# Performance work log

Hardware: AMD Instinct MI355X
Metric: run time of the kernel (lower is better)

Reference implementation:

```python
import jax, jax.numpy as jnp
import numpy as np

B, H, L, N, COND = 8, 128, 16384, 16, 4  # N = s4_hidden_size // 2 complex states (conjugate symmetry)
BN_EPS = 1e-5


def setup_inputs() -> dict:
    key = jax.random.key(0)
    ks = jax.random.split(key, 12)
    x = jax.random.normal(ks[0], (B, H, L), jnp.float32)
    conditional_information = jax.random.normal(ks[1], (B, COND), jnp.float32)
    # input linear (H -> H)
    lin_w = jax.random.normal(ks[2], (H, H), jnp.float32) / np.sqrt(H)
    lin_b = jnp.zeros((H,), jnp.float32)
    prelu1_a = jnp.array(0.25, jnp.float32)
    # S4D (diag) parameters, ZOH discretization, S4D-Lin init
    u = jax.random.uniform(ks[3], (H,), jnp.float32)
    log_dt = np.log(1e-3) + u * (np.log(1e-1) - np.log(1e-3))  # [H]
    log_A_real = jnp.log(0.5 * jnp.ones((H, N), jnp.float32))
    A_imag = jnp.broadcast_to(np.pi * jnp.arange(N, dtype=jnp.float32), (H, N)).copy()
    C_re = jax.random.normal(ks[4], (H, N), jnp.float32)
    C_im = jax.random.normal(ks[5], (H, N), jnp.float32)
    D = jax.random.normal(ks[6], (H,), jnp.float32)
    out_w = jax.random.normal(ks[7], (H, H), jnp.float32) / np.sqrt(H)
    out_b = jnp.zeros((H,), jnp.float32)
    # FiLM: cond -> (gamma, beta) per channel
    film_w = jax.random.normal(ks[8], (2 * H, COND), jnp.float32) / np.sqrt(COND)
    film_b = jnp.zeros((2 * H,), jnp.float32)
    prelu2_a = jnp.array(0.25, jnp.float32)
    # depthwise 1x1 conv residual: per-channel scale
    res_w = jax.random.normal(ks[9], (H,), jnp.float32) / np.sqrt(H)
    return dict(x=x, conditional_information=conditional_information,
                lin_w=lin_w, lin_b=lin_b, prelu1_a=prelu1_a,
                log_dt=log_dt, log_A_real=log_A_real, A_imag=A_imag,
                C_re=C_re, C_im=C_im, D=D, out_w=out_w, out_b=out_b,
                film_w=film_w, film_b=film_b, prelu2_a=prelu2_a, res_w=res_w)


def _prelu(v, a):
    return jnp.where(v > 0, v, a * v)


def _s4d(u, log_dt, log_A_real, A_imag, C_re, C_im, D, out_w, out_b):
    # u: [B, H, L]. Diagonal SSM kernel via Vandermonde + FFT convolution (ZOH).
    Lx = u.shape[-1]
    dt = jnp.exp(log_dt)                                   # [H]
    A = -jnp.exp(log_A_real) + 1j * A_imag                 # [H, N] complex
    dtA = dt[:, None] * A                                  # [H, N]
    dB = (jnp.exp(dtA) - 1.0) / A                          # ZOH: (e^{dtA}-1)/A, B=1
    Ceff = (C_re + 1j * C_im) * dB                         # [H, N]
    t = jnp.arange(Lx, dtype=jnp.float32)
    vand = jnp.exp(dtA[:, :, None] * t)                    # [H, N, L] = (e^{dtA})^l
    K = 2.0 * jnp.real(jnp.einsum('hn,hnl->hl', Ceff, vand))  # [H, L]
    n = 2 * Lx
    y = jnp.fft.irfft(jnp.fft.rfft(u, n) * jnp.fft.rfft(K, n)[None], n)[..., :Lx]
    y = y + D[None, :, None] * u
    # position-wise output linear (activation='id')
    return jnp.einsum('bhl,gh->bgl', y, out_w) + out_b[None, :, None]


def reference(x, conditional_information, lin_w, lin_b, prelu1_a,
              log_dt, log_A_real, A_imag, C_re, C_im, D, out_w, out_b,
              film_w, film_b, prelu2_a, res_w):
    out = jnp.einsum('bhl,gh->bgl', x, lin_w) + lin_b[None, :, None]
    out = _prelu(out, prelu1_a)
    out = _s4d(out, log_dt, log_A_real, A_imag, C_re, C_im, D, out_w, out_b)
    # BatchNorm1d(affine=False), training-mode statistics over (B, L)
    mean = jnp.mean(out, axis=(0, 2), keepdims=True)
    var = jnp.var(out, axis=(0, 2), keepdims=True)
    out = (out - mean) * jax.lax.rsqrt(var + BN_EPS)
    # FiLM
    gb = conditional_information @ film_w.T + film_b       # [B, 2H]
    g, b = gb[:, :H], gb[:, H:]
    out = out * g[:, :, None] + b[:, :, None]
    out = _prelu(out, prelu2_a)
    # depthwise 1x1 conv residual (groups=H, no bias): per-channel scale of x
    return out + res_w[None, :, None] * x
```

## Files before the change

kernel.cpp:

```cpp
#include <hip/hip_runtime.h>
#include <math.h>

#define B_ 8
#define H_ 128
#define L_ 16384
#define N_ 16
#define CHUNK_ 64
#define NCH_ 256

typedef float f32x4 __attribute__((ext_vector_type(4)));
typedef short bf16x8 __attribute__((ext_vector_type(8)));

static __device__ __forceinline__ unsigned int f2bf(float f) {
  unsigned int u = __float_as_uint(f);
  return (u + 0x7FFFu + ((u >> 16) & 1u)) >> 16;
}
static __device__ __forceinline__ float bf2f(unsigned int us) {
  return __uint_as_float(us << 16);
}

__global__ __launch_bounds__(256) void prep2_kernel(
    const float* __restrict__ lin_w, const float* __restrict__ out_w,
    const float* __restrict__ log_dt, const float* __restrict__ log_A_real,
    const float* __restrict__ A_imag, const float* __restrict__ C_re,
    const float* __restrict__ C_im, const float* __restrict__ cond,
    const float* __restrict__ film_w, const float* __restrict__ film_b,
    unsigned short* __restrict__ wA16, unsigned short* __restrict__ wB16,
    float* __restrict__ consts,
    float* __restrict__ gact, float* __restrict__ bact)
{
  int blk = blockIdx.x, t = threadIdx.x;
  if (blk < 16) {
    int base = blk * 1024;
    #pragma unroll
    for (int it = 0; it < 4; it++) {
      int i = base + it * 256 + t;
      wA16[i] = (unsigned short)f2bf(lin_w[i]);
      wB16[i] = (unsigned short)f2bf(out_w[i]);
    }
  } else if (blk == 16) {
    for (int i = t; i < H_ * N_; i += 256) {
      int h = i >> 4, n = i & 15;
      float dt  = expf(log_dt[h]);
      float Are = -expf(log_A_real[i]);
      float Aim = A_imag[i];
      float dre = dt * Are, dim = dt * Aim;
      float er  = expf(dre);
      float wre = er * cosf(dim);
      float wim = er * sinf(dim);
      float den = Are * Are + Aim * Aim;
      float nre = wre - 1.0f, nim = wim;
      float dBre = (nre * Are + nim * Aim) / den;
      float dBim = (nim * Are - nre * Aim) / den;
      float cr = C_re[i], ci = C_im[i];
      float cere = cr * dBre - ci * dBim;
      float ceim = cr * dBim + ci * dBre;
      float e2   = expf((float)CHUNK_ * dre);
      float wcre = e2 * cosf((float)CHUNK_ * dim);
      float wcim = e2 * sinf((float)CHUNK_ * dim);
      float* cb = consts + h * 96;
      cb[n]      = wre;  cb[16 + n] = wim;
      cb[32 + n] = cere; cb[48 + n] = ceim;
      cb[64 + n] = wcre; cb[80 + n] = wcim;
    }
  } else {
    for (int i = t; i < B_ * 2 * H_; i += 256) {
      int b = i >> 8, k = i & 255;
      float acc = film_b[k];
      #pragma unroll
      for (int c = 0; c < 4; c++) acc += cond[b * 4 + c] * film_w[k * 4 + c];
      if (k < H_) gact[b * H_ + k] = acc;
      else        bact[b * H_ + (k - H_)] = acc;
    }
  }
}

template<int MODE>
__global__ __launch_bounds__(256) void mgemm_kernel(
    const void* inv, const unsigned short* __restrict__ w16,
    const float* __restrict__ bias, const float* __restrict__ prelu_a,
    unsigned short* __restrict__ outb)
{
  __shared__ __align__(16) unsigned short xT[64 * 128];
  char* xb = (char*)xT;
  int tid = threadIdx.x;
  int blk = blockIdx.x;
  int b   = blk >> 8;
  int jb  = (blk & 255) << 6;

  {
    int hp = tid >> 4;
    int jq = tid & 15;
    int h0 = hp << 3;
    if (MODE == 0) {
      const float* inb = (const float*)inv + ((size_t)b * H_) * L_ + jb;
      f32x4 r[8];
      #pragma unroll
      for (int rr = 0; rr < 8; rr++)
        r[rr] = *reinterpret_cast<const f32x4*>(&inb[(size_t)(h0 + rr) * L_ + (jq << 2)]);
      #pragma unroll
      for (int jj = 0; jj < 4; jj++) {
        int j = (jq << 2) + jj;
        uint4 pk;
        pk.x = f2bf(r[0][jj]) | (f2bf(r[1][jj]) << 16);
        pk.y = f2bf(r[2][jj]) | (f2bf(r[3][jj]) << 16);
        pk.z = f2bf(r[4][jj]) | (f2bf(r[5][jj]) << 16);
        pk.w = f2bf(r[6][jj]) | (f2bf(r[7][jj]) << 16);
        int addr = j * 256 + ((hp << 4) ^ ((j & 15) << 4));
        *reinterpret_cast<uint4*>(xb + addr) = pk;
      }
    } else {
      const unsigned short* ub = (const unsigned short*)inv;
      uint2 rv[8];
      #pragma unroll
      for (int rr = 0; rr < 8; rr++)
        rv[rr] = *reinterpret_cast<const uint2*>(
            ub + ((size_t)(b * H_ + h0 + rr)) * 32768 + jb + (jq << 2));
      #pragma unroll
      for (int jj = 0; jj < 4; jj++) {
        int j = (jq << 2) + jj;
        uint4 pk;
        #define EXT_(v) ((((jj & 2) ? (v).y : (v).x) >> ((jj & 1) << 4)) & 0xFFFFu)
        pk.x = EXT_(rv[0]) | (EXT_(rv[1]) << 16);
        pk.y = EXT_(rv[2]) | (EXT_(rv[3]) << 16);
        pk.z = EXT_(rv[4]) | (EXT_(rv[5]) << 16);
        pk.w = EXT_(rv[6]) | (EXT_(rv[7]) << 16);
        #undef EXT_
        int addr = j * 256 + ((hp << 4) ^ ((j & 15) << 4));
        *reinterpret_cast<uint4*>(xb + addr) = pk;
      }
    }
  }
  __syncthreads();

  int lane = tid & 63;
  int w    = tid >> 6;
  int wg   = w >> 1;
  int wj   = w & 1;
  int ln   = lane & 15;
  int q    = lane >> 4;
  f32x4 acc[4][2];
  #pragma unroll
  for (int mi = 0; mi < 4; mi++)
    #pragma unroll
    for (int n = 0; n < 2; n++) acc[mi][n] = (f32x4)0.0f;

  #pragma unroll
  for (int kb = 0; kb < 4; kb++) {
    bf16x8 a[4], bv[2];
    #pragma unroll
    for (int mi = 0; mi < 4; mi++)
      a[mi] = *reinterpret_cast<const bf16x8*>(
          &w16[(size_t)(wg * 64 + mi * 16 + ln) * 128 + kb * 32 + q * 8]);
    #pragma unroll
    for (int n = 0; n < 2; n++) {
      int jl = wj * 32 + n * 16 + ln;
      int ar = jl * 256 + (((kb << 6) + (q << 4)) ^ ((jl & 15) << 4));
      bv[n] = *reinterpret_cast<bf16x8*>(xb + ar);
    }
    #pragma unroll
    for (int mi = 0; mi < 4; mi++)
      #pragma unroll
      for (int n = 0; n < 2; n++)
        acc[mi][n] = __builtin_amdgcn_mfma_f32_16x16x32_bf16(a[mi], bv[n], acc[mi][n], 0, 0, 0);
  }

  float pa = (MODE == 0) ? prelu_a[0] : 0.0f;
  #pragma unroll
  for (int mi = 0; mi < 4; mi++) {
    #pragma unroll
    for (int r = 0; r < 4; r++) {
      int g = wg * 64 + mi * 16 + q * 4 + r;
      float bvs = bias[g];
      float v0 = acc[mi][0][r] + bvs;
      float v1 = acc[mi][1][r] + bvs;
      if (MODE == 0) {
        v0 = (v0 > 0.0f) ? v0 : pa * v0;
        v1 = (v1 > 0.0f) ? v1 : pa * v1;
      }
      size_t ob = ((size_t)(b * H_ + g)) * 32768 + jb + wj * 32 + ln;
      outb[ob]      = (unsigned short)f2bf(v0);
      outb[ob + 16] = (unsigned short)f2bf(v1);
    }
  }
}

__global__ __launch_bounds__(1024) void scan3_kernel(
    unsigned short* ub, const float* __restrict__ consts, const float* __restrict__ Dp)
{
  __shared__ unsigned int rowl[8192];
  __shared__ float st[NCH_ * 36];
  int tid = threadIdx.x;
  int row = blockIdx.x;
  int h   = row & 127;
  const float* cb = consts + h * 96;
  unsigned int* grow = (unsigned int*)ub + (size_t)row * 16384;

  #pragma unroll
  for (int rd = 0; rd < 2; rd++) {
    int u0  = rd * 4096 + tid * 4;
    uint4 v = *reinterpret_cast<const uint4*>(grow + u0);
    int x   = (u0 >> 5) & 31;
    int bse = u0 ^ (x & ~3);
    int pl  = x & 3;
    if (pl & 1) v = make_uint4(v.y, v.x, v.w, v.z);
    if (pl & 2) v = make_uint4(v.z, v.w, v.x, v.y);
    *reinterpret_cast<uint4*>(&rowl[bse]) = v;
  }
  __syncthreads();

  int c   = tid >> 2;
  int m   = tid & 3;
  int swz = c & 31;
  unsigned int* rc = rowl + c * 32;
  float* sc = st + c * 36 + m * 8;

  float wre[4], wim[4];
  #pragma unroll
  for (int k = 0; k < 4; k++) { wre[k] = cb[4*m+k]; wim[k] = cb[16+4*m+k]; }

  float sre[4] = {0.f,0.f,0.f,0.f}, sim[4] = {0.f,0.f,0.f,0.f};

  for (int e = 0; e < 32; e++) {
    unsigned int pv = rc[e ^ swz];
    float u0 = bf2f(pv & 0xFFFFu), u1 = bf2f(pv >> 16);
    #pragma unroll
    for (int k = 0; k < 4; k++) {
      float nr = fmaf(wre[k], sre[k], fmaf(-wim[k], sim[k], u0));
      float ni = fmaf(wre[k], sim[k], wim[k] * sre[k]);
      sre[k] = nr; sim[k] = ni;
    }
    #pragma unroll
    for (int k = 0; k < 4; k++) {
      float nr = fmaf(wre[k], sre[k], fmaf(-wim[k], sim[k], u1));
      float ni = fmaf(wre[k], sim[k], wim[k] * sre[k]);
      sre[k] = nr; sim[k] = ni;
    }
  }
  #pragma unroll
  for (int k = 0; k < 4; k++) { sc[2*k] = sre[k]; sc[2*k+1] = sim[k]; }
  __syncthreads();

  {
    float mre[4], mim[4];
    #pragma unroll
    for (int k = 0; k < 4; k++) { mre[k] = cb[64+4*m+k]; mim[k] = cb[80+4*m+k]; }
    for (int s = 0; s < 8; s++) {
      int off = 1 << s;
      float pr[4], pi[4];
      bool act = (c >= off);
      if (act) {
        const float* pc = st + (c - off) * 36 + m * 8;
        #pragma unroll
        for (int k = 0; k < 4; k++) { pr[k] = pc[2*k]; pi[k] = pc[2*k+1]; }
      }
      __syncthreads();
      if (act) {
        #pragma unroll
        for (int k = 0; k < 4; k++) {
          sre[k] = fmaf(mre[k], pr[k], fmaf(-mim[k], pi[k], sre[k]));
          sim[k] = fmaf(mre[k], pi[k], fmaf( mim[k], pr[k], sim[k]));
        }
        #pragma unroll
        for (int k = 0; k < 4; k++) { sc[2*k] = sre[k]; sc[2*k+1] = sim[k]; }
      }
      if (s < 7) {
        #pragma unroll
        for (int k = 0; k < 4; k++) {
          float r = mre[k], i2 = mim[k];
          mre[k] = r * r - i2 * i2;
          mim[k] = 2.0f * r * i2;
        }
      }
      __syncthreads();
    }
  }

  float cre[4], cim[4];
  #pragma unroll
  for (int k = 0; k < 4; k++) { cre[k] = cb[32+4*m+k]; cim[k] = cb[48+4*m+k]; }
  float Dv = Dp[h];
  if (c == 0) {
    #pragma unroll
    for (int k = 0; k < 4; k++) { sre[k] = 0.0f; sim[k] = 0.0f; }
  } else {
    const float* pc = st + (c - 1) * 36 + m * 8;
    #pragma unroll
    for (int k = 0; k < 4; k++) { sre[k] = pc[2*k]; sim[k] = pc[2*k+1]; }
  }
  for (int e = 0; e < 32; e++) {
    int p = e ^ swz;
    unsigned int pv = rc[p];
    float u0 = bf2f(pv & 0xFFFFu), u1 = bf2f(pv >> 16);
    float y0 = 0.0f, y1 = 0.0f;
    #pragma unroll
    for (int k = 0; k < 4; k++) {
      float nr = fmaf(wre[k], sre[k], fmaf(-wim[k], sim[k], u0));
      float ni = fmaf(wre[k], sim[k], wim[k] * sre[k]);
      sre[k] = nr; sim[k] = ni;
      y0 = fmaf(cre[k], nr, fmaf(-cim[k], ni, y0));
    }
    #pragma unroll
    for (int k = 0; k < 4; k++) {
      float nr = fmaf(wre[k], sre[k], fmaf(-wim[k], sim[k], u1));
      float ni = fmaf(wre[k], sim[k], wim[k] * sre[k]);
      sre[k] = nr; sim[k] = ni;
      y1 = fmaf(cre[k], nr, fmaf(-cim[k], ni, y1));
    }
    y0 += __shfl_xor(y0, 1); y0 += __shfl_xor(y0, 2);
    y1 += __shfl_xor(y1, 1); y1 += __shfl_xor(y1, 2);
    if (m == 0) {
      y0 = fmaf(Dv, u0, 2.0f * y0);
      y1 = fmaf(Dv, u1, 2.0f * y1);
      rc[p] = f2bf(y0) | (f2bf(y1) << 16);
    }
  }
  __syncthreads();

  #pragma unroll
  for (int rd = 0; rd < 2; rd++) {
    int u0  = rd * 4096 + tid * 4;
    int x   = (u0 >> 5) & 31;
    int bse = u0 ^ (x & ~3);
    int pl  = x & 3;
    uint4 v = *reinterpret_cast<const uint4*>(&rowl[bse]);
    if (pl & 1) v = make_uint4(v.y, v.x, v.w, v.z);
    if (pl & 2) v = make_uint4(v.z, v.w, v.x, v.y);
    *reinterpret_cast<uint4*>(grow + u0) = v;
  }
}

__global__ __launch_bounds__(256) void stats1_kernel(
    const unsigned short* __restrict__ ub,
    float* __restrict__ sums, float* __restrict__ sumsq)
{
  int row = blockIdx.x, tid = threadIdx.x;
  const unsigned int* zr = (const unsigned int*)ub + (size_t)row * 16384;
  float s1 = 0.0f, s2 = 0.0f;
  #pragma unroll
  for (int rd = 0; rd < 8; rd++) {
    uint4 v = *reinterpret_cast<const uint4*>(zr + rd * 1024 + tid * 4);
    unsigned int ws_[4] = {v.x, v.y, v.z, v.w};
    #pragma unroll
    for (int k = 0; k < 4; k++) {
      float f0 = bf2f(ws_[k] & 0xFFFFu), f1 = bf2f(ws_[k] >> 16);
      s1 += f0 + f1;
      s2 = fmaf(f0, f0, fmaf(f1, f1, s2));
    }
  }
  #pragma unroll
  for (int off = 1; off < 64; off <<= 1) {
    s1 += __shfl_xor(s1, off);
    s2 += __shfl_xor(s2, off);
  }
  __shared__ float a1[4], a2[4];
  int wv = tid >> 6;
  if ((tid & 63) == 0) { a1[wv] = s1; a2[wv] = s2; }
  __syncthreads();
  if (tid == 0) {
    sums[row]  = a1[0] + a1[1] + a1[2] + a1[3];
    sumsq[row] = a2[0] + a2[1] + a2[2] + a2[3];
  }
}

__global__ void stats2_kernel(const float* __restrict__ sums,
                              const float* __restrict__ sumsq,
                              float* __restrict__ meanp, float* __restrict__ invp)
{
  int g = threadIdx.x;
  if (g < H_) {
    double s1 = 0.0, s2 = 0.0;
    #pragma unroll
    for (int b = 0; b < B_; b++) {
      s1 += (double)sums[b * H_ + g];
      s2 += (double)sumsq[b * H_ + g];
    }
    double cnt = (double)B_ * (double)L_;
    double mu  = s1 / cnt;
    double var = s2 / cnt - mu * mu;
    meanp[g] = (float)mu;
    invp[g]  = (float)(1.0 / sqrt(var + 1e-5));
  }
}

__global__ __launch_bounds__(256) void final2_kernel(
    unsigned short* __restrict__ ub, float* __restrict__ outf,
    const float* __restrict__ x,
    const float* __restrict__ meanp, const float* __restrict__ invp,
    const float* __restrict__ gact, const float* __restrict__ bact,
    const float* __restrict__ prelu2_a, const float* __restrict__ res_w)
{
  int row = blockIdx.x, tid = threadIdx.x;
  int b = row >> 7, g = row & 127;
  const unsigned int* zr = (const unsigned int*)ub + (size_t)row * 16384;
  uint4 zq0 = *reinterpret_cast<const uint4*>(zr + 0 * 1024 + tid * 4);
  uint4 zq1 = *reinterpret_cast<const uint4*>(zr + 1 * 1024 + tid * 4);
  uint4 zq2 = *reinterpret_cast<const uint4*>(zr + 2 * 1024 + tid * 4);
  uint4 zq3 = *reinterpret_cast<const uint4*>(zr + 3 * 1024 + tid * 4);
  uint4 zq4 = *reinterpret_cast<const uint4*>(zr + 4 * 1024 + tid * 4);
  uint4 zq5 = *reinterpret_cast<const uint4*>(zr + 5 * 1024 + tid * 4);
  uint4 zq6 = *reinterpret_cast<const uint4*>(zr + 6 * 1024 + tid * 4);
  uint4 zq7 = *reinterpret_cast<const uint4*>(zr + 7 * 1024 + tid * 4);
  __syncthreads();

  float m  = meanp[g], iv = invp[g];
  float ga = gact[b * H_ + g], bb = bact[b * H_ + g];
  float rw = res_w[g], pa = prelu2_a[0];
  const float* xr = x + (size_t)row * L_;
  float* orow = outf + (size_t)row * L_;

  uint4 zqa[8] = {zq0, zq1, zq2, zq3, zq4, zq5, zq6, zq7};
  #pragma unroll
  for (int rd = 0; rd < 8; rd++) {
    int e0 = rd * 2048 + tid * 8;
    f32x4 x0 = *reinterpret_cast<const f32x4*>(xr + e0);
    f32x4 x1 = *reinterpret_cast<const f32x4*>(xr + e0 + 4);
    unsigned int wz[4] = {zqa[rd].x, zqa[rd].y, zqa[rd].z, zqa[rd].w};
    f32x4 o0, o1;
    #pragma unroll
    for (int k = 0; k < 4; k++) {
      float z0 = bf2f(wz[k] & 0xFFFFu), z1 = bf2f(wz[k] >> 16);
      float v0 = fmaf((z0 - m) * iv, ga, bb);
      float v1 = fmaf((z1 - m) * iv, ga, bb);
      v0 = (v0 > 0.0f) ? v0 : pa * v0;
      v1 = (v1 > 0.0f) ? v1 : pa * v1;
      float xa = (k < 2) ? x0[2 * k] : x1[2 * k - 4];
      float xbv = (k < 2) ? x0[2 * k + 1] : x1[2 * k - 3];
      float r0 = fmaf(rw, xa, v0);
      float r1 = fmaf(rw, xbv, v1);
      if (k < 2) { o0[2 * k] = r0; o0[2 * k + 1] = r1; }
      else       { o1[2 * k - 4] = r0; o1[2 * k - 3] = r1; }
    }
    *reinterpret_cast<f32x4*>(orow + e0)     = o0;
    *reinterpret_cast<f32x4*>(orow + e0 + 4) = o1;
  }
}

extern "C" void kernel_launch(void* const* d_in, const int* in_sizes, int n_in,
                              void* d_out, int out_size, void* d_ws, size_t ws_size,
                              hipStream_t stream)
{
  const float* x        = (const float*)d_in[0];
  const float* cond     = (const float*)d_in[1];
  const float* lin_w    = (const float*)d_in[2];
  const float* lin_b    = (const float*)d_in[3];
  const float* prelu1_a = (const float*)d_in[4];
  const float* log_dt   = (const float*)d_in[5];
  const float* log_A    = (const float*)d_in[6];
  const float* A_imag   = (const float*)d_in[7];
  const float* C_re     = (const float*)d_in[8];
  const float* C_im     = (const float*)d_in[9];
  const float* Dp       = (const float*)d_in[10];
  const float* out_w    = (const float*)d_in[11];
  const float* out_b    = (const float*)d_in[12];
  const float* film_w   = (const float*)d_in[13];
  const float* film_b   = (const float*)d_in[14];
  const float* prelu2_a = (const float*)d_in[15];
  const float* res_w    = (const float*)d_in[16];
  float* outf = (float*)d_out;
  unsigned short* ubuf = (unsigned short*)d_out;

  char* wsb = (char*)d_ws;
  float* consts         = (float*)(wsb + 0);
  unsigned short* wA16  = (unsigned short*)(wsb + 49152);
  unsigned short* wB16  = (unsigned short*)(wsb + 81920);
  float* gact           = (float*)(wsb + 114688);
  float* bact           = (float*)(wsb + 118784);
  float* meanp          = (float*)(wsb + 122880);
  float* invp           = (float*)(wsb + 123392);
  float* sums           = (float*)(wsb + 123904);
  float* sumsq          = (float*)(wsb + 128000);

  prep2_kernel<<<18, 256, 0, stream>>>(lin_w, out_w, log_dt, log_A, A_imag, C_re, C_im,
                                       cond, film_w, film_b, wA16, wB16, consts, gact, bact);
  mgemm_kernel<0><<<2048, 256, 0, stream>>>(x, wA16, lin_b, prelu1_a, ubuf);
  scan3_kernel<<<1024, 1024, 0, stream>>>(ubuf, consts, Dp);
  mgemm_kernel<1><<<2048, 256, 0, stream>>>(ubuf, wB16, out_b, nullptr, ubuf);
  stats1_kernel<<<1024, 256, 0, stream>>>(ubuf, sums, sumsq);
  stats2_kernel<<<1, 128, 0, stream>>>(sums, sumsq, meanp, invp);
  final2_kernel<<<1024, 256, 0, stream>>>(ubuf, outf, x, meanp, invp, gact, bact,
                                          prelu2_a, res_w);
}
```

Measured before the change: 331.8 us.

## Rewrite chunk scan with wave shuffles and widen GEMM tiles to 128 columns

The scan kernel's cross-chunk prefix now runs in two levels. Inside each wave it uses __shfl_up in four steps, and a small shared aggregate combines waves. This replaces the previous eight-step shared-memory scan that needed two block barriers per step. The LDS swizzle is simplified and each thread reads two bf16 pairs per iteration. Separately, the bf16 GEMM kernels process 128 sequence columns per block instead of 64, which halves the grid and doubles the MFMA work per wave, at the cost of more registers and twice the LDS.

```diff
diff --git a/kernel.cpp b/kernel.cpp
--- a/kernel.cpp
+++ b/kernel.cpp
@@ -81,51 +81,59 @@
     const float* __restrict__ bias, const float* __restrict__ prelu_a,
     unsigned short* __restrict__ outb)
 {
-  __shared__ __align__(16) unsigned short xT[64 * 128];
+  __shared__ __align__(16) unsigned short xT[128 * 128];
   char* xb = (char*)xT;
   int tid = threadIdx.x;
   int blk = blockIdx.x;
-  int b   = blk >> 8;
-  int jb  = (blk & 255) << 6;
+  int b   = blk >> 7;
+  int jb  = (blk & 127) << 7;
 
   {
     int hp = tid >> 4;
     int jq = tid & 15;
     int h0 = hp << 3;
+    int j0 = jq << 3;
     if (MODE == 0) {
       const float* inb = (const float*)inv + ((size_t)b * H_) * L_ + jb;
-      f32x4 r[8];
-      #pragma unroll
-      for (int rr = 0; rr < 8; rr++)
-        r[rr] = *reinterpret_cast<const f32x4*>(&inb[(size_t)(h0 + rr) * L_ + (jq << 2)]);
-      #pragma unroll
-      for (int jj = 0; jj < 4; jj++) {
-        int j = (jq << 2) + jj;
+      f32x4 r[8][2];
+      #pragma unroll
+      for (int rr = 0; rr < 8; rr++) {
+        r[rr][0] = *reinterpret_cast<const f32x4*>(&inb[(size_t)(h0 + rr) * L_ + j0]);
+        r[rr][1] = *reinterpret_cast<const f32x4*>(&inb[(size_t)(h0 + rr) * L_ + j0 + 4]);
+      }
+      #pragma unroll
+      for (int jj = 0; jj < 8; jj++) {
+        int j = j0 + jj;
         uint4 pk;
-        pk.x = f2bf(r[0][jj]) | (f2bf(r[1][jj]) << 16);
-        pk.y = f2bf(r[2][jj]) | (f2bf(r[3][jj]) << 16);
-        pk.z = f2bf(r[4][jj]) | (f2bf(r[5][jj]) << 16);
-        pk.w = f2bf(r[6][jj]) | (f2bf(r[7][jj]) << 16);
+        #define GE_(rr) ((jj < 4) ? r[rr][0][jj] : r[rr][1][jj - 4])
+        pk.x = f2bf(GE_(0)) | (f2bf(GE_(1)) << 16);
+        pk.y = f2bf(GE_(2)) | (f2bf(GE_(3)) << 16);
+        pk.z = f2bf(GE_(4)) | (f2bf(GE_(5)) << 16);
+        pk.w = f2bf(GE_(6)) | (f2bf(GE_(7)) << 16);
+        #undef GE_
         int addr = j * 256 + ((hp << 4) ^ ((j & 15) << 4));
         *reinterpret_cast<uint4*>(xb + addr) = pk;
       }
     } else {
       const unsigned short* ub = (const unsigned short*)inv;
-      uint2 rv[8];
+      uint4 rv[8];
       #pragma unroll
       for (int rr = 0; rr < 8; rr++)
-        rv[rr] = *reinterpret_cast<const uint2*>(
-            ub + ((size_t)(b * H_ + h0 + rr)) * 32768 + jb + (jq << 2));
-      #pragma unroll
-      for (int jj = 0; jj < 4; jj++) {
-        int j = (jq << 2) + jj;
+        rv[rr] = *reinterpret_cast<const uint4*>(
+            ub + ((size_t)(b * H_ + h0 + rr)) * 32768 + jb + j0);
+      #pragma unroll
+      for (int jj = 0; jj < 8; jj++) {
+        int j = j0 + jj;
         uint4 pk;
-        #define EXT_(v) ((((jj & 2) ? (v).y : (v).x) >> ((jj & 1) << 4)) & 0xFFFFu)
-        pk.x = EXT_(rv[0]) | (EXT_(rv[1]) << 16);
-        pk.y = EXT_(rv[2]) | (EXT_(rv[3]) << 16);
-        pk.z = EXT_(rv[4]) | (EXT_(rv[5]) << 16);
-        pk.w = EXT_(rv[6]) | (EXT_(rv[7]) << 16);
+        #define WD_(rr) ((jj >> 1) == 0 ? rv[rr].x : (jj >> 1) == 1 ? rv[rr].y : \
+                         (jj >> 1) == 2 ? rv[rr].z : rv[rr].w)
+        #define EXT_(rr) (((jj & 1) ? (WD_(rr) >> 16) : WD_(rr)) & 0xFFFFu)
+        pk.x = EXT_(0) | (EXT_(1) << 16);
+        pk.y = EXT_(2) | (EXT_(3) << 16);
+        pk.z = EXT_(4) | (EXT_(5) << 16);
+        pk.w = EXT_(6) | (EXT_(7) << 16);
         #undef EXT_
+        #undef WD_
         int addr = j * 256 + ((hp << 4) ^ ((j & 15) << 4));
         *reinterpret_cast<uint4*>(xb + addr) = pk;
       }
@@ -139,29 +147,29 @@
   int wj   = w & 1;
   int ln   = lane & 15;
   int q    = lane >> 4;
-  f32x4 acc[4][2];
+  f32x4 acc[4][4];
   #pragma unroll
   for (int mi = 0; mi < 4; mi++)
     #pragma unroll
-    for (int n = 0; n < 2; n++) acc[mi][n] = (f32x4)0.0f;
+    for (int n = 0; n < 4; n++) acc[mi][n] = (f32x4)0.0f;
 
   #pragma unroll
   for (int kb = 0; kb < 4; kb++) {
-    bf16x8 a[4], bv[2];
+    bf16x8 a[4], bv[4];
     #pragma unroll
     for (int mi = 0; mi < 4; mi++)
       a[mi] = *reinterpret_cast<const bf16x8*>(
           &w16[(size_t)(wg * 64 + mi * 16 + ln) * 128 + kb * 32 + q * 8]);
     #pragma unroll
-    for (int n = 0; n < 2; n++) {
-      int jl = wj * 32 + n * 16 + ln;
+    for (int n = 0; n < 4; n++) {
+      int jl = wj * 64 + n * 16 + ln;
       int ar = jl * 256 + (((kb << 6) + (q << 4)) ^ ((jl & 15) << 4));
       bv[n] = *reinterpret_cast<bf16x8*>(xb + ar);
     }
     #pragma unroll
     for (int mi = 0; mi < 4; mi++)
       #pragma unroll
-      for (int n = 0; n < 2; n++)
+      for (int n = 0; n < 4; n++)
         acc[mi][n] = __builtin_amdgcn_mfma_f32_16x16x32_bf16(a[mi], bv[n], acc[mi][n], 0, 0, 0);
   }
 
@@ -172,24 +180,22 @@
     for (int r = 0; r < 4; r++) {
       int g = wg * 64 + mi * 16 + q * 4 + r;
       float bvs = bias[g];
-      float v0 = acc[mi][0][r] + bvs;
-      float v1 = acc[mi][1][r] + bvs;
-      if (MODE == 0) {
-        v0 = (v0 > 0.0f) ? v0 : pa * v0;
-        v1 = (v1 > 0.0f) ? v1 : pa * v1;
+      size_t orow = ((size_t)(b * H_ + g)) * 32768 + jb + wj * 64 + ln;
+      #pragma unroll
+      for (int n = 0; n < 4; n++) {
+        float v = acc[mi][n][r] + bvs;
+        if (MODE == 0) v = (v > 0.0f) ? v : pa * v;
+        outb[orow + n * 16] = (unsigned short)f2bf(v);
       }
-      size_t ob = ((size_t)(b * H_ + g)) * 32768 + jb + wj * 32 + ln;
-      outb[ob]      = (unsigned short)f2bf(v0);
-      outb[ob + 16] = (unsigned short)f2bf(v1);
-    }
-  }
-}
-
-__global__ __launch_bounds__(1024) void scan3_kernel(
+    }
+  }
+}
+
+__global__ __launch_bounds__(1024) void scan4_kernel(
     unsigned short* ub, const float* __restrict__ consts, const float* __restrict__ Dp)
 {
   __shared__ unsigned int rowl[8192];
-  __shared__ float st[NCH_ * 36];
+  __shared__ float agg[16][32];
   int tid = threadIdx.x;
   int row = blockIdx.x;
   int h   = row & 127;
@@ -198,22 +204,20 @@
 
   #pragma unroll
   for (int rd = 0; rd < 2; rd++) {
-    int u0  = rd * 4096 + tid * 4;
-    uint4 v = *reinterpret_cast<const uint4*>(grow + u0);
-    int x   = (u0 >> 5) & 31;
-    int bse = u0 ^ (x & ~3);
-    int pl  = x & 3;
-    if (pl & 1) v = make_uint4(v.y, v.x, v.w, v.z);
-    if (pl & 2) v = make_uint4(v.z, v.w, v.x, v.y);
-    *reinterpret_cast<uint4*>(&rowl[bse]) = v;
+    int u0   = rd * 4096 + tid * 4;
+    uint4 v  = *reinterpret_cast<const uint4*>(grow + u0);
+    int phys = u0 ^ (((u0 >> 5) & 7) << 2);
+    *reinterpret_cast<uint4*>(&rowl[phys]) = v;
   }
   __syncthreads();
 
-  int c   = tid >> 2;
-  int m   = tid & 3;
-  int swz = c & 31;
-  unsigned int* rc = rowl + c * 32;
-  float* sc = st + c * 36 + m * 8;
+  int c     = tid >> 2;
+  int m     = tid & 3;
+  int lane  = tid & 63;
+  int cl    = lane >> 2;
+  int wv    = tid >> 6;
+  int cbase = c * 32;
+  int swz   = (c & 7) << 2;
 
   float wre[4], wim[4];
   #pragma unroll
@@ -221,111 +225,134 @@
 
   float sre[4] = {0.f,0.f,0.f,0.f}, sim[4] = {0.f,0.f,0.f,0.f};
 
-  for (int e = 0; e < 32; e++) {
-    unsigned int pv = rc[e ^ swz];
-    float u0 = bf2f(pv & 0xFFFFu), u1 = bf2f(pv >> 16);
-    #pragma unroll
-    for (int k = 0; k < 4; k++) {
-      float nr = fmaf(wre[k], sre[k], fmaf(-wim[k], sim[k], u0));
-      float ni = fmaf(wre[k], sim[k], wim[k] * sre[k]);
-      sre[k] = nr; sim[k] = ni;
-    }
-    #pragma unroll
-    for (int k = 0; k < 4; k++) {
-      float nr = fmaf(wre[k], sre[k], fmaf(-wim[k], sim[k], u1));
-      float ni = fmaf(wre[k], sim[k], wim[k] * sre[k]);
-      sre[k] = nr; sim[k] = ni;
-    }
-  }
-  #pragma unroll
-  for (int k = 0; k < 4; k++) { sc[2*k] = sre[k]; sc[2*k+1] = sim[k]; }
+  #define UPD_(uval) { \
+    _Pragma("unroll") \
+    for (int k = 0; k < 4; k++) { \
+      float nr = fmaf(wre[k], sre[k], fmaf(-wim[k], sim[k], (uval))); \
+      float ni = fmaf(wre[k], sim[k], wim[k] * sre[k]); \
+      sre[k] = nr; sim[k] = ni; } }
+
+  for (int e2 = 0; e2 < 16; e2++) {
+    int idx  = (cbase + 2 * e2) ^ swz;
+    uint2 pv = *reinterpret_cast<uint2*>(&rowl[idx]);
+    float u0 = __uint_as_float(pv.x << 16);
+    float u1 = __uint_as_float(pv.x & 0xFFFF0000u);
+    float u2 = __uint_as_float(pv.y << 16);
+    float u3 = __uint_as_float(pv.y & 0xFFFF0000u);
+    UPD_(u0); UPD_(u1); UPD_(u2); UPD_(u3);
+  }
+
+  float mre[4], mim[4];
+  #pragma unroll
+  for (int k = 0; k < 4; k++) { mre[k] = cb[64+4*m+k]; mim[k] = cb[80+4*m+k]; }
+  float pwr[4] = {1.f,1.f,1.f,1.f}, pwi[4] = {0.f,0.f,0.f,0.f};
+  #pragma unroll
+  for (int s = 0; s < 4; s++) {
+    int off = 1 << s;
+    bool bit = (cl >> s) & 1;
+    #pragma unroll
+    for (int k = 0; k < 4; k++) {
+      float tr = fmaf(pwr[k], mre[k], -(pwi[k] * mim[k]));
+      float ti = fmaf(pwr[k], mim[k],  (pwi[k] * mre[k]));
+      pwr[k] = bit ? tr : pwr[k];
+      pwi[k] = bit ? ti : pwi[k];
+    }
+    bool act = (cl >= off);
+    #pragma unroll
+    for (int k = 0; k < 4; k++) {
+      float pr = __shfl_up(sre[k], 4 * off, 64);
+      float pi = __shfl_up(sim[k], 4 * off, 64);
+      float nr = fmaf(mre[k], pr, fmaf(-mim[k], pi, sre[k]));
+      float ni = fmaf(mre[k], pi, fmaf( mim[k], pr, sim[k]));
+      sre[k] = act ? nr : sre[k];
+      sim[k] = act ? ni : sim[k];
+    }
+    #pragma unroll
+    for (int k = 0; k < 4; k++) {
+      float r = mre[k], i2 = mim[k];
+      mre[k] = fmaf(r, r, -(i2 * i2));
+      mim[k] = 2.0f * r * i2;
+    }
+  }
+
+  if (cl == 15) {
+    #pragma unroll
+    for (int k = 0; k < 4; k++) {
+      agg[wv][m * 8 + 2 * k]     = sre[k];
+      agg[wv][m * 8 + 2 * k + 1] = sim[k];
+    }
+  }
   __syncthreads();
-
-  {
-    float mre[4], mim[4];
-    #pragma unroll
-    for (int k = 0; k < 4; k++) { mre[k] = cb[64+4*m+k]; mim[k] = cb[80+4*m+k]; }
-    for (int s = 0; s < 8; s++) {
-      int off = 1 << s;
-      float pr[4], pi[4];
-      bool act = (c >= off);
-      if (act) {
-        const float* pc = st + (c - off) * 36 + m * 8;
-        #pragma unroll
-        for (int k = 0; k < 4; k++) { pr[k] = pc[2*k]; pi[k] = pc[2*k+1]; }
-      }
-      __syncthreads();
-      if (act) {
-        #pragma unroll
-        for (int k = 0; k < 4; k++) {
-          sre[k] = fmaf(mre[k], pr[k], fmaf(-mim[k], pi[k], sre[k]));
-          sim[k] = fmaf(mre[k], pi[k], fmaf( mim[k], pr[k], sim[k]));
-        }
-        #pragma unroll
-        for (int k = 0; k < 4; k++) { sc[2*k] = sre[k]; sc[2*k+1] = sim[k]; }
-      }
-      if (s < 7) {
-        #pragma unroll
-        for (int k = 0; k < 4; k++) {
-          float r = mre[k], i2 = mim[k];
-          mre[k] = r * r - i2 * i2;
-          mim[k] = 2.0f * r * i2;
-        }
-      }
-      __syncthreads();
-    }
+  float Cr[4] = {0.f,0.f,0.f,0.f}, Ci[4] = {0.f,0.f,0.f,0.f};
+  for (int wp = 0; wp < wv; wp++) {
+    #pragma unroll
+    for (int k = 0; k < 4; k++) {
+      float ar = agg[wp][m * 8 + 2 * k];
+      float ai = agg[wp][m * 8 + 2 * k + 1];
+      float nr = fmaf(mre[k], Cr[k], fmaf(-mim[k], Ci[k], ar));
+      float ni = fmaf(mre[k], Ci[k], fmaf( mim[k], Cr[k], ai));
+      Cr[k] = nr; Ci[k] = ni;
+    }
+  }
+
+  #pragma unroll
+  for (int k = 0; k < 4; k++) {
+    float er = __shfl_up(sre[k], 4, 64);
+    float ei = __shfl_up(sim[k], 4, 64);
+    float br = (cl == 0) ? 0.0f : er;
+    float bi = (cl == 0) ? 0.0f : ei;
+    sre[k] = fmaf(pwr[k], Cr[k], fmaf(-pwi[k], Ci[k], br));
+    sim[k] = fmaf(pwr[k], Ci[k], fmaf( pwi[k], Cr[k], bi));
   }
 
   float cre[4], cim[4];
   #pragma unroll
   for (int k = 0; k < 4; k++) { cre[k] = cb[32+4*m+k]; cim[k] = cb[48+4*m+k]; }
   float Dv = Dp[h];
-  if (c == 0) {
-    #pragma unroll
-    for (int k = 0; k < 4; k++) { sre[k] = 0.0f; sim[k] = 0.0f; }
-  } else {
-    const float* pc = st + (c - 1) * 36 + m * 8;
-    #pragma unroll
-    for (int k = 0; k < 4; k++) { sre[k] = pc[2*k]; sim[k] = pc[2*k+1]; }
-  }
-  for (int e = 0; e < 32; e++) {
-    int p = e ^ swz;
-    unsigned int pv = rc[p];
-    float u0 = bf2f(pv & 0xFFFFu), u1 = bf2f(pv >> 16);
-    float y0 = 0.0f, y1 = 0.0f;
-    #pragma unroll
-    for (int k = 0; k < 4; k++) {
-      float nr = fmaf(wre[k], sre[k], fmaf(-wim[k], sim[k], u0));
-      float ni = fmaf(wre[k], sim[k], wim[k] * sre[k]);
-      sre[k] = nr; sim[k] = ni;
-      y0 = fmaf(cre[k], nr, fmaf(-cim[k], ni, y0));
-    }
-    #pragma unroll
-    for (int k = 0; k < 4; k++) {
-      float nr = fmaf(wre[k], sre[k], fmaf(-wim[k], sim[k], u1));
-      float ni = fmaf(wre[k], sim[k], wim[k] * sre[k]);
-      sre[k] = nr; sim[k] = ni;
-      y1 = fmaf(cre[k], nr, fmaf(-cim[k], ni, y1));
-    }
+
+  #define STEP_(uval, yout) { \
+    float ya = 0.0f; \
+    _Pragma("unroll") \
+    for (int k = 0; k < 4; k++) { \
+      float nr = fmaf(wre[k], sre[k], fmaf(-wim[k], sim[k], (uval))); \
+      float ni = fmaf(wre[k], sim[k], wim[k] * sre[k]); \
+      sre[k] = nr; sim[k] = ni; \
+      ya = fmaf(cre[k], nr, fmaf(-cim[k], ni, ya)); } \
+    yout = ya; }
+
+  for (int e2 = 0; e2 < 16; e2++) {
+    int idx  = (cbase + 2 * e2) ^ swz;
+    uint2 pv = *reinterpret_cast<uint2*>(&rowl[idx]);
+    float u0 = __uint_as_float(pv.x << 16);
+    float u1 = __uint_as_float(pv.x & 0xFFFF0000u);
+    float u2 = __uint_as_float(pv.y << 16);
+    float u3 = __uint_as_float(pv.y & 0xFFFF0000u);
+    float y0, y1, y2, y3;
+    STEP_(u0, y0); STEP_(u1, y1); STEP_(u2, y2); STEP_(u3, y3);
     y0 += __shfl_xor(y0, 1); y0 += __shfl_xor(y0, 2);
     y1 += __shfl_xor(y1, 1); y1 += __shfl_xor(y1, 2);
+    y2 += __shfl_xor(y2, 1); y2 += __shfl_xor(y2, 2);
+    y3 += __shfl_xor(y3, 1); y3 += __shfl_xor(y3, 2);
     if (m == 0) {
       y0 = fmaf(Dv, u0, 2.0f * y0);
       y1 = fmaf(Dv, u1, 2.0f * y1);
-      rc[p] = f2bf(y0) | (f2bf(y1) << 16);
-    }
-  }
+      y2 = fmaf(Dv, u2, 2.0f * y2);
+      y3 = fmaf(Dv, u3, 2.0f * y3);
+      uint2 pk;
+      pk.x = f2bf(y0) | (f2bf(y1) << 16);
+      pk.y = f2bf(y2) | (f2bf(y3) << 16);
+      *reinterpret_cast<uint2*>(&rowl[idx]) = pk;
+    }
+  }
+  #undef UPD_
+  #undef STEP_
   __syncthreads();
 
   #pragma unroll
   for (int rd = 0; rd < 2; rd++) {
-    int u0  = rd * 4096 + tid * 4;
-    int x   = (u0 >> 5) & 31;
-    int bse = u0 ^ (x & ~3);
-    int pl  = x & 3;
-    uint4 v = *reinterpret_cast<const uint4*>(&rowl[bse]);
-    if (pl & 1) v = make_uint4(v.y, v.x, v.w, v.z);
-    if (pl & 2) v = make_uint4(v.z, v.w, v.x, v.y);
+    int u0   = rd * 4096 + tid * 4;
+    int phys = u0 ^ (((u0 >> 5) & 7) << 2);
+    uint4 v  = *reinterpret_cast<const uint4*>(&rowl[phys]);
     *reinterpret_cast<uint4*>(grow + u0) = v;
   }
 }
@@ -473,9 +500,9 @@
 
   prep2_kernel<<<18, 256, 0, stream>>>(lin_w, out_w, log_dt, log_A, A_imag, C_re, C_im,
                                        cond, film_w, film_b, wA16, wB16, consts, gact, bact);
-  mgemm_kernel<0><<<2048, 256, 0, stream>>>(x, wA16, lin_b, prelu1_a, ubuf);
-  scan3_kernel<<<1024, 1024, 0, stream>>>(ubuf, consts, Dp);
-  mgemm_kernel<1><<<2048, 256, 0, stream>>>(ubuf, wB16, out_b, nullptr, ubuf);
+  mgemm_kernel<0><<<1024, 256, 0, stream>>>(x, wA16, lin_b, prelu1_a, ubuf);
+  scan4_kernel<<<1024, 1024, 0, stream>>>(ubuf, consts, Dp);
+  mgemm_kernel<1><<<1024, 256, 0, stream>>>(ubuf, wB16, out_b, nullptr, ubuf);
   stats1_kernel<<<1024, 256, 0, stream>>>(ubuf, sums, sumsq);
   stats2_kernel<<<1, 128, 0, stream>>>(sums, sumsq, meanp, invp);
   final2_kernel<<<1024, 256, 0, stream>>>(ubuf, outf, x, meanp, invp, gact, bact,
```

Result: faster. 314.6 us (-5.2%).
